# Optimization experiments

Measured on AMD Instinct MI355X. Metric: run time of the kernel, lower is better.

Reference implementation:

```python
import jax, jax.numpy as jnp
import numpy as np
import math

B, N, DIM, H, DH, NNULL = 2, 2048, 1024, 16, 64, 2
SCALE = 8.0
LN_EPS = 1e-5


def _alibi_slopes(heads):
    # heads is a power of 2 here (16): slopes = start * start**i
    start = 2.0 ** (-(2.0 ** (-(math.log2(heads) - 3))))
    return np.array([start * (start ** i) for i in range(heads)], dtype=np.float32)


def setup_inputs() -> dict:
    key = jax.random.key(0)
    ks = jax.random.split(key, 6)
    inner = H * DH
    return {
        "x": jax.random.normal(ks[0], (B, N, DIM), dtype=jnp.float32),
        "norm_g": jnp.ones((DIM,), jnp.float32),
        "norm_b": jnp.zeros((DIM,), jnp.float32),
        "Wq": jax.random.normal(ks[1], (DIM, inner), jnp.float32) * 0.02,
        "Wkv": jax.random.normal(ks[2], (DIM, 2 * inner), jnp.float32) * 0.02,
        "q_scale": jnp.ones((DH,), jnp.float32),
        "k_scale": jnp.ones((DH,), jnp.float32),
        "null_kv": jax.random.normal(ks[3], (H, 2 * NNULL, DH), jnp.float32),
        "Wout": jax.random.normal(ks[4], (inner, DIM), jnp.float32) * 0.02,
    }


def _l2norm(t):
    # matches F.normalize: x / max(||x||, 1e-12)
    n = jnp.sqrt(jnp.sum(t * t, axis=-1, keepdims=True))
    return t / jnp.maximum(n, 1e-12)


def reference(x, norm_g, norm_b, Wq, Wkv, q_scale, k_scale, null_kv, Wout):
    b, n, dim = x.shape
    h, dh, nn = H, DH, NNULL
    j = n + nn

    # NOTE: faithful to source -- K/V come from the PRE-norm x (kv_input bound
    # before x = self.norm(x)); only Q uses the LayerNorm'd x.
    mu = jnp.mean(x, axis=-1, keepdims=True)
    var = jnp.mean((x - mu) ** 2, axis=-1, keepdims=True)
    xn = (x - mu) * jax.lax.rsqrt(var + LN_EPS) * norm_g + norm_b

    q = (xn @ Wq).reshape(b, n, h, dh).transpose(0, 2, 1, 3)          # b h n d
    kv = x @ Wkv
    k, v = jnp.split(kv, 2, axis=-1)
    k = k.reshape(b, n, h, dh).transpose(0, 2, 1, 3)                   # b h n d
    v = v.reshape(b, n, h, dh).transpose(0, 2, 1, 3)

    # null kv: (h, 2*nn, dh) -> (h, nn, 2, dh)
    null = null_kv.reshape(h, nn, 2, dh)
    nk = jnp.broadcast_to(null[:, :, 0, :][None], (b, h, nn, dh))
    nv = jnp.broadcast_to(null[:, :, 1, :][None], (b, h, nn, dh))
    k = jnp.concatenate([nk, k], axis=2)                               # b h j d
    v = jnp.concatenate([nv, v], axis=2)

    q = _l2norm(q) * q_scale
    k = _l2norm(k) * k_scale

    sim = jnp.einsum('bhid,bhjd->bhij', q, k) * SCALE                  # b h n j

    # ALiBi bias: rows at positions j-n..j-1, cols 0..j-1
    irow = jnp.arange(j - n, j)
    jcol = jnp.arange(j)
    bias = -jnp.abs(jcol[None, :] - irow[:, None]).astype(sim.dtype)   # (n, j)
    slopes = jnp.asarray(_alibi_slopes(h))[:, None, None]              # (h,1,1)
    sim = sim + slopes * bias

    # causal mask: triu with offset j - n + 1 (null kv always visible)
    causal = jnp.triu(jnp.ones((n, j), dtype=bool), k=j - n + 1)
    neg = jnp.finfo(sim.dtype).max
    sim = jnp.where(causal[None, None], -neg, sim)

    attn = jax.nn.softmax(sim, axis=-1)
    out = jnp.einsum('bhij,bhjd->bhid', attn, v)
    out = out.transpose(0, 2, 1, 3).reshape(b, n, h * dh)
    return out @ Wout
```

## Files before the change

### kernel.cpp

```cpp
#include <hip/hip_runtime.h>
#include <hip/hip_bf16.h>
#include <stdint.h>

#define H_    16
#define N_    2048
#define DIM_  1024
#define DH_   64
#define NN_   2
#define J_    2050
#define JP_   2112
#define B_    2
#define M_    4096
#define NSEG_ 84

#define S8L_  11.541560327111707f
#define LOG2E_ 1.4426950408889634f

typedef unsigned short u16;
typedef unsigned int u32;
typedef short bf16x8 __attribute__((ext_vector_type(8)));
typedef float f32x4 __attribute__((ext_vector_type(4)));

__device__ __forceinline__ u16 f2b(float f) {
  union { float f; unsigned int i; } v; v.f = f;
  unsigned int r = v.i + 0x7fffu + ((v.i >> 16) & 1u);
  return (u16)(r >> 16);
}
__device__ __forceinline__ float b2f(u16 u) {
  union { unsigned int i; float f; } v; v.i = ((unsigned int)u) << 16; return v.f;
}
__device__ __forceinline__ float lo2f(u32 u) {
  union { u32 i; float f; } v; v.i = u << 16; return v.f;
}
__device__ __forceinline__ float hi2f(u32 u) {
  union { u32 i; float f; } v; v.i = u & 0xffff0000u; return v.f;
}
__device__ __forceinline__ void unp8(const uint4 u, float* d) {
  d[0] = lo2f(u.x); d[1] = hi2f(u.x); d[2] = lo2f(u.y); d[3] = hi2f(u.y);
  d[4] = lo2f(u.z); d[5] = hi2f(u.z); d[6] = lo2f(u.w); d[7] = hi2f(u.w);
}
__device__ __forceinline__ u32 pk2(float a, float b) {
  union { __hip_bfloat162 h; u32 u; } x;
  x.h = __float22bfloat162_rn(make_float2(a, b));
  return x.u;
}
__device__ __forceinline__ void dma16(const u16* g, u16* l) {
  __builtin_amdgcn_global_load_lds(
      (const __attribute__((address_space(1))) u32*)(const void*)g,
      (__attribute__((address_space(3))) u32*)(void*)l, 16, 0, 0);
}

__global__ __launch_bounds__(256) void ktranspose_cast(const float* __restrict__ in,
                                                       u16* __restrict__ out, int R, int C) {
  __shared__ float tile[32][33];
  int tx = threadIdx.x & 31, ty = threadIdx.x >> 5;
  int c0 = blockIdx.x * 32, r0 = blockIdx.y * 32;
  #pragma unroll
  for (int i = 0; i < 32; i += 8)
    tile[ty + i][tx] = in[(size_t)(r0 + ty + i) * C + c0 + tx];
  __syncthreads();
  #pragma unroll
  for (int i = 0; i < 32; i += 8)
    out[(size_t)(c0 + ty + i) * R + r0 + tx] = f2b(tile[tx][ty + i]);
}

__global__ __launch_bounds__(256) void lnorm_k(const float* __restrict__ x,
                                               const float* __restrict__ g,
                                               const float* __restrict__ bb,
                                               u16* __restrict__ xn,
                                               u16* __restrict__ xbf) {
  int row = blockIdx.x;
  int t = threadIdx.x;
  float4 rw = *(const float4*)(x + (size_t)row * DIM_ + t * 4);
  float v0 = rw.x, v1 = rw.y, v2 = rw.z, v3 = rw.w;
  uint2 cw;
  cw.x = pk2(v0, v1);
  cw.y = pk2(v2, v3);
  *(uint2*)(xbf + (size_t)row * DIM_ + t * 4) = cw;
  float s = v0 + v1 + v2 + v3;
  float ss = v0 * v0 + v1 * v1 + v2 * v2 + v3 * v3;
  #pragma unroll
  for (int o = 32; o; o >>= 1) { s += __shfl_xor(s, o, 64); ss += __shfl_xor(ss, o, 64); }
  __shared__ float red[8];
  int lane = t & 63, w = t >> 6;
  if (lane == 0) { red[w] = s; red[4 + w] = ss; }
  __syncthreads();
  float S = red[0] + red[1] + red[2] + red[3];
  float SS = red[4] + red[5] + red[6] + red[7];
  float mu = S * (1.0f / DIM_);
  float var = SS * (1.0f / DIM_) - mu * mu;
  float rs = rsqrtf(var + 1e-5f);
  float4 gv = *(const float4*)(g + t * 4);
  float4 bv = *(const float4*)(bb + t * 4);
  uint2 ow;
  ow.x = pk2((v0 - mu) * rs * gv.x + bv.x, (v1 - mu) * rs * gv.y + bv.y);
  ow.y = pk2((v2 - mu) * rs * gv.z + bv.z, (v3 - mu) * rs * gv.w + bv.w);
  *(uint2*)(xn + (size_t)row * DIM_ + t * 4) = ow;
}

template <int MODE>
__global__ __launch_bounds__(256) void gemm_k(const u16* __restrict__ A,
                                              const u16* __restrict__ BT,
                                              void* __restrict__ dst0,
                                              void* __restrict__ dst1,
                                              const float* __restrict__ scale,
                                              int M, int Nc, int K) {
  __shared__ u16 As[128 * 64];
  __shared__ u16 Bs[64 * 64];
  int tid = threadIdx.x, wv = tid >> 6, lane = tid & 63;
  int fm = lane & 15, fg = lane >> 4;
  int row0 = blockIdx.y * 128, col0 = blockIdx.x * 64;
  f32x4 acc[2][4] = {};
  int srow = lane >> 3;
  int skb = ((lane & 7) ^ srow) * 8;
  const u16* Ag = A + (size_t)(row0 + wv * 32 + srow) * K + skb;
  const u16* Bg = BT + (size_t)(col0 + wv * 16 + srow) * K + skb;
  u16* AsW = As + (wv * 32) * 64;
  u16* BsW = Bs + (wv * 16) * 64;
  int fr7 = fm & 7;
  int ak0 = (fg ^ fr7) * 8;
  int ak1 = ((fg + 4) ^ fr7) * 8;
  for (int k0 = 0; k0 < K; k0 += 64) {
    __syncthreads();
    dma16(Ag + k0,                    AsW);
    dma16(Ag + (size_t)8 * K + k0,    AsW + 8 * 64);
    dma16(Ag + (size_t)16 * K + k0,   AsW + 16 * 64);
    dma16(Ag + (size_t)24 * K + k0,   AsW + 24 * 64);
    dma16(Bg + k0,                    BsW);
    dma16(Bg + (size_t)8 * K + k0,    BsW + 8 * 64);
    __syncthreads();
    bf16x8 af0[2], af1[2], bf0[4], bf1[4];
    #pragma unroll
    for (int mt = 0; mt < 2; mt++) {
      int rbase = (wv * 32 + mt * 16 + fm) * 64;
      af0[mt] = *(const bf16x8*)&As[rbase + ak0];
      af1[mt] = *(const bf16x8*)&As[rbase + ak1];
    }
    #pragma unroll
    for (int nt = 0; nt < 4; nt++) {
      int rbase = (nt * 16 + fm) * 64;
      bf0[nt] = *(const bf16x8*)&Bs[rbase + ak0];
      bf1[nt] = *(const bf16x8*)&Bs[rbase + ak1];
    }
    #pragma unroll
    for (int mt = 0; mt < 2; mt++)
      #pragma unroll
      for (int nt = 0; nt < 4; nt++) {
        acc[mt][nt] = __builtin_amdgcn_mfma_f32_16x16x32_bf16(af0[mt], bf0[nt], acc[mt][nt], 0, 0, 0);
        acc[mt][nt] = __builtin_amdgcn_mfma_f32_16x16x32_bf16(af1[mt], bf1[nt], acc[mt][nt], 0, 0, 0);
      }
  }
  if (MODE == 1) {
    float* C = (float*)dst0;
    #pragma unroll
    for (int mt = 0; mt < 2; mt++)
      #pragma unroll
      for (int r = 0; r < 4; r++) {
        int m = row0 + wv * 32 + mt * 16 + fg * 4 + r;
        #pragma unroll
        for (int nt = 0; nt < 4; nt++)
          C[(size_t)m * Nc + col0 + nt * 16 + fm] = acc[mt][nt][r];
      }
  } else {
    bool isK = (MODE == 2) || (col0 < 1024);
    int h = (isK ? col0 : col0 - 1024) >> 6;
    float sv[4];
    if (isK) {
      #pragma unroll
      for (int nt = 0; nt < 4; nt++) sv[nt] = scale[nt * 16 + fm];
      if (MODE == 2) {
        #pragma unroll
        for (int nt = 0; nt < 4; nt++) sv[nt] *= S8L_;
      }
    }
    u16* Do = (u16*)((MODE == 3 && !isK) ? dst1 : dst0);
    #pragma unroll
    for (int mt = 0; mt < 2; mt++) {
      #pragma unroll
      for (int r = 0; r < 4; r++) {
        float inv = 1.0f;
        if (isK) {
          float ssp = 0.0f;
          #pragma unroll
          for (int nt = 0; nt < 4; nt++) ssp += acc[mt][nt][r] * acc[mt][nt][r];
          #pragma unroll
          for (int o = 1; o <= 8; o <<= 1) ssp += __shfl_xor(ssp, o, 64);
          inv = 1.0f / fmaxf(sqrtf(ssp), 1e-12f);
        }
        int m = row0 + wv * 32 + mt * 16 + fg * 4 + r;
        int b = m >> 11, n = m & 2047;
        size_t base;
        if (MODE == 2)      base = (((size_t)(b * H_ + h)) * N_ + n) * 64;
        else if (isK)       base = (((size_t)(b * H_ + h)) * JP_ + (n + NN_)) * 64;
        else                base = (((size_t)(b * H_ + h)) * J_ + (n + NN_)) * 64;
        #pragma unroll
        for (int nt = 0; nt < 4; nt++) {
          float val = acc[mt][nt][r];
          if (isK) val = val * inv * sv[nt];
          Do[base + nt * 16 + fm] = f2b(val);
        }
      }
    }
  }
}

__global__ __launch_bounds__(256) void vtransp_k(const u16* __restrict__ Vb,
                                                 const float* __restrict__ nkv,
                                                 const float* __restrict__ ks,
                                                 u16* __restrict__ Kb,
                                                 u16* __restrict__ VTp) {
  __shared__ u16 tile[64][80];
  int t = threadIdx.x;
  int c = blockIdx.x, bh = blockIdx.y, h = bh & 15;
  int jl = t >> 2, dc = (t & 3) * 16;
  int j = c * 64 + jl;
  if (j < NN_) {
    float kvv[16];
    float kssp = 0.0f;
    #pragma unroll
    for (int e = 0; e < 16; e++) {
      float vv = nkv[(size_t)(h * 4 + 2 * j + 1) * 64 + dc + e];
      tile[jl][dc + e] = f2b(vv);
      float kv = nkv[(size_t)(h * 4 + 2 * j) * 64 + dc + e];
      kvv[e] = kv; kssp += kv * kv;
    }
    kssp += __shfl_xor(kssp, 1, 64);
    kssp += __shfl_xor(kssp, 2, 64);
    float inv = 1.0f / fmaxf(sqrtf(kssp), 1e-12f);
    #pragma unroll
    for (int e = 0; e < 16; e++)
      Kb[((size_t)bh * JP_ + j) * 64 + dc + e] = f2b(kvv[e] * inv * ks[dc + e]);
  } else if (j < J_) {
    const uint4* src = (const uint4*)(Vb + ((size_t)bh * J_ + j) * 64 + dc);
    *(uint4*)&tile[jl][dc] = src[0];
    *(uint4*)&tile[jl][dc + 8] = src[1];
  } else {
    uint4 z = {0, 0, 0, 0};
    *(uint4*)&tile[jl][dc] = z;
    *(uint4*)&tile[jl][dc + 8] = z;
  }
  __syncthreads();
  int d = t >> 2, p0 = (t & 3) * 16;
  u16 tmp[16] __attribute__((aligned(16)));
  #pragma unroll
  for (int e = 0; e < 16; e++) {
    int pos = p0 + e;
    int h2 = pos >> 5, rem = pos & 31;
    int fgp = rem >> 3, tt = rem & 7;
    int nt = tt >> 2, r = tt & 3;
    int jloc = (h2 * 2 + nt) * 16 + fgp * 4 + r;
    tmp[e] = tile[jloc][d];
  }
  uint4* dstp = (uint4*)(VTp + ((size_t)bh * 64 + d) * JP_ + c * 64 + p0);
  dstp[0] = ((uint4*)tmp)[0];
  dstp[1] = ((uint4*)tmp)[1];
}

__global__ __launch_bounds__(256, 6) void attn_k(const u16* __restrict__ Qn,
                                                 const u16* __restrict__ Kb,
                                                 const u16* __restrict__ VTp,
                                                 const float* __restrict__ qs,
                                                 const float* __restrict__ ks,
                                                 u16* __restrict__ partials) {
  __shared__ u16 Ks0[64 * 32], Ks1[64 * 32];
  __shared__ u16 Vs0[64 * 32], Vs1[64 * 32];
  int tid = threadIdx.x;
  int wv = tid >> 6, lane = tid & 63;
  int fm = lane & 15, fg = lane >> 4;
  int n = (int)blockIdx.x + NSEG_ * (int)blockIdx.y;
  int m = n >> 3;
  int bh = (n & 7) * 4 + m / NSEG_;
  int segid = m % NSEG_;
  int h = bh & 15;
  int cum = 0, qt = 0, seg = 0;
  #pragma unroll 1
  for (int i = 0; i < 32; i++) {
    int t = 31 - i, s = (t + 9) >> 3;
    if (segid < cum + s) { qt = t; seg = segid - cum; break; }
    cum += s;
  }
  int q0 = qt * 64;
  int q = q0 + wv * 16 + fm;
  float slope = exp2f(-0.5f * (float)(h + 1));
  float prod = fabsf(qs[lane] * ks[lane]);
  #pragma unroll
  for (int o = 32; o; o >>= 1) prod = fmaxf(prod, __shfl_xor(prod, o, 64));
  float MbL = 8.0f * prod * LOG2E_;
  float slopeL = slope * LOG2E_;
  const u16* qp = Qn + ((size_t)bh * N_ + q) * 64 + fg * 8;
  bf16x8 qf0 = *(const bf16x8*)(qp);
  bf16x8 qf1 = *(const bf16x8*)(qp + 32);
  f32x4 accO[4] = {};
  float lp = 0.0f;
  int lr = lane >> 2;
  int kbs = ((lane & 3) ^ ((lane >> 3) & 3)) * 8;
  int fs = (fg ^ ((fm >> 1) & 3)) * 8;
  const u16* KbBH = Kb + (size_t)bh * JP_ * 64;
  const u16* VTbh = VTp + (size_t)bh * 64 * JP_;
  int c0 = seg * 8;
  int c1 = min(c0 + 8, qt + 2);
  float bias0 = slopeL * (float)(c0 * 64 + fg * 4 - q - 2) - MbL;
  float sr1 = slopeL, sr2 = slopeL * 2.0f, sr3 = slopeL * 3.0f;
  float s16 = slopeL * 16.0f;
  float d64 = slopeL * 64.0f;
  for (int c = c0; c < c1; c++) {
    int jb = c * 64;
    __syncthreads();
    const u16* Kg = KbBH + (size_t)(jb + wv * 16 + lr) * 64 + kbs;
    dma16(Kg,      Ks0 + wv * 512);
    dma16(Kg + 32, Ks1 + wv * 512);
    const u16* Vg = VTbh + (size_t)(wv * 16 + lr) * JP_ + jb + kbs;
    dma16(Vg,      Vs0 + wv * 512);
    dma16(Vg + 32, Vs1 + wv * 512);
    __syncthreads();
    f32x4 accS[4] = {};
    #pragma unroll
    for (int nt = 0; nt < 4; nt++) {
      bf16x8 kf0 = *(const bf16x8*)&Ks0[(nt * 16 + fm) * 32 + fs];
      accS[nt] = __builtin_amdgcn_mfma_f32_16x16x32_bf16(kf0, qf0, accS[nt], 0, 0, 0);
      bf16x8 kf1 = *(const bf16x8*)&Ks1[(nt * 16 + fm) * 32 + fs];
      accS[nt] = __builtin_amdgcn_mfma_f32_16x16x32_bf16(kf1, qf1, accS[nt], 0, 0, 0);
    }
    union { bf16x8 v; u32 u[4]; } P0, P1;
    float lps = 0.0f;
    float bnt = bias0;
    if (c < qt) {
      #pragma unroll
      for (int nt = 0; nt < 4; nt++) {
        float e0 = __builtin_amdgcn_exp2f(accS[nt][0] + bnt);
        float e1 = __builtin_amdgcn_exp2f((accS[nt][1] + sr1) + bnt);
        float e2 = __builtin_amdgcn_exp2f((accS[nt][2] + sr2) + bnt);
        float e3 = __builtin_amdgcn_exp2f((accS[nt][3] + sr3) + bnt);
        u32 w0 = pk2(e0, e1);
        u32 w1 = pk2(e2, e3);
        lps += (e0 + e1) + (e2 + e3);
        if (nt < 2) { P0.u[nt * 2] = w0; P0.u[nt * 2 + 1] = w1; }
        else        { P1.u[(nt - 2) * 2] = w0; P1.u[(nt - 2) * 2 + 1] = w1; }
        bnt += s16;
      }
    } else {
      int thr = q + 2 - jb;
      #pragma unroll
      for (int nt = 0; nt < 4; nt++) {
        int ib = nt * 16 + fg * 4;
        float e0 = __builtin_amdgcn_exp2f(accS[nt][0] + bnt);
        float e1 = __builtin_amdgcn_exp2f((accS[nt][1] + sr1) + bnt);
        float e2 = __builtin_amdgcn_exp2f((accS[nt][2] + sr2) + bnt);
        float e3 = __builtin_amdgcn_exp2f((accS[nt][3] + sr3) + bnt);
        e0 = (ib + 0 <= thr) ? e0 : 0.0f;
        e1 = (ib + 1 <= thr) ? e1 : 0.0f;
        e2 = (ib + 2 <= thr) ? e2 : 0.0f;
        e3 = (ib + 3 <= thr) ? e3 : 0.0f;
        u32 w0 = pk2(e0, e1);
        u32 w1 = pk2(e2, e3);
        lps += (e0 + e1) + (e2 + e3);
        if (nt < 2) { P0.u[nt * 2] = w0; P0.u[nt * 2 + 1] = w1; }
        else        { P1.u[(nt - 2) * 2] = w0; P1.u[(nt - 2) * 2 + 1] = w1; }
        bnt += s16;
      }
    }
    lp += lps;
    bias0 += d64;
    #pragma unroll
    for (int nt = 0; nt < 4; nt++) {
      bf16x8 vf0 = *(const bf16x8*)&Vs0[(nt * 16 + fm) * 32 + fs];
      accO[nt] = __builtin_amdgcn_mfma_f32_16x16x32_bf16(vf0, P0.v, accO[nt], 0, 0, 0);
      bf16x8 vf1 = *(const bf16x8*)&Vs1[(nt * 16 + fm) * 32 + fs];
      accO[nt] = __builtin_amdgcn_mfma_f32_16x16x32_bf16(vf1, P1.v, accO[nt], 0, 0, 0);
    }
  }
  lp += __shfl_xor(lp, 16, 64);
  lp += __shfl_xor(lp, 32, 64);
  u16* P = partials + ((size_t)bh * NSEG_ + segid) * 4224;
  int sq = wv * 16 + fm;
  #pragma unroll
  for (int nt = 0; nt < 4; nt++) {
    uint2 ow;
    ow.x = pk2(accO[nt][0], accO[nt][1]);
    ow.y = pk2(accO[nt][2], accO[nt][3]);
    *(uint2*)(P + sq * 64 + nt * 16 + fg * 4) = ow;
  }
  if (fg == 0) *(float*)(P + 4096 + 2 * sq) = lp;
}

__global__ __launch_bounds__(256) void comb_k(const u16* __restrict__ partials,
                                              u16* __restrict__ AO) {
  int qt = blockIdx.x, bh = blockIdx.y, b = bh >> 4, h = bh & 15;
  int t = threadIdx.x, q = t >> 2, dq = (t & 3) * 16;
  int s = (qt + 9) >> 3;
  int cum = 0;
  for (int tt = qt + 1; tt < 32; tt++) cum += (tt + 9) >> 3;
  float acc[16] = {};
  float lsum = 0.0f;
  for (int k = 0; k < s; k++) {
    const u16* P = partials + ((size_t)bh * NSEG_ + cum + k) * 4224;
    uint4 a = *(const uint4*)(P + q * 64 + dq);
    uint4 bq = *(const uint4*)(P + q * 64 + dq + 8);
    float tmp[8];
    unp8(a, tmp);
    #pragma unroll
    for (int e = 0; e < 8; e++) acc[e] += tmp[e];
    unp8(bq, tmp);
    #pragma unroll
    for (int e = 0; e < 8; e++) acc[8 + e] += tmp[e];
    lsum += *(const float*)(P + 4096 + 2 * q);
  }
  float linv = 1.0f / lsum;
  int n = qt * 64 + q;
  u16* dst = AO + (((size_t)(b * N_ + n)) * H_ + h) * 64 + dq;
  u16 ov[16] __attribute__((aligned(16)));
  #pragma unroll
  for (int e = 0; e < 16; e++) ov[e] = f2b(acc[e] * linv);
  *(uint4*)dst = ((uint4*)ov)[0];
  *(uint4*)(dst + 8) = ((uint4*)ov)[1];
}

extern "C" void kernel_launch(void* const* d_in, const int* in_sizes, int n_in,
                              void* d_out, int out_size, void* d_ws, size_t ws_size,
                              hipStream_t stream) {
  const float* x    = (const float*)d_in[0];
  const float* ng   = (const float*)d_in[1];
  const float* nb   = (const float*)d_in[2];
  const float* Wq   = (const float*)d_in[3];
  const float* Wkv  = (const float*)d_in[4];
  const float* qs   = (const float*)d_in[5];
  const float* ks   = (const float*)d_in[6];
  const float* nkv  = (const float*)d_in[7];
  const float* Wout = (const float*)d_in[8];
  float* out = (float*)d_out;
  char* ws = (char*)d_ws;

  u16* xn    = (u16*)(ws + 0);
  u16* WoutT = (u16*)(ws + 8388608);
  u16* Qn    = (u16*)(ws + 10485760);
  u16* Kb    = (u16*)(ws + 18874368);
  u16* VTp   = (u16*)(ws + 27525120);
  u16* xbf   = (u16*)(ws + 36175872);
  u16* WqT   = (u16*)(ws + 44564480);
  u16* WkvT  = (u16*)(ws + 46661632);
  u16* Vb    = (u16*)(ws + 50855936);
  u16* parts = xbf;
  u16* AO    = xn;

  hipMemsetAsync(Kb, 0, 8650752, stream);
  ktranspose_cast<<<dim3(32, 32), 256, 0, stream>>>(Wq, WqT, 1024, 1024);
  ktranspose_cast<<<dim3(64, 32), 256, 0, stream>>>(Wkv, WkvT, 1024, 2048);
  ktranspose_cast<<<dim3(32, 32), 256, 0, stream>>>(Wout, WoutT, 1024, 1024);
  lnorm_k<<<4096, 256, 0, stream>>>(x, ng, nb, xn, xbf);
  gemm_k<2><<<dim3(16, 32), 256, 0, stream>>>(xn, WqT, Qn, nullptr, qs, M_, 1024, 1024);
  gemm_k<3><<<dim3(32, 32), 256, 0, stream>>>(xbf, WkvT, Kb, Vb, ks, M_, 2048, 1024);
  vtransp_k<<<dim3(33, 32), 256, 0, stream>>>(Vb, nkv, ks, Kb, VTp);
  attn_k<<<dim3(NSEG_, 32), 256, 0, stream>>>(Qn, Kb, VTp, qs, ks, parts);
  comb_k<<<dim3(32, 32), 256, 0, stream>>>(parts, AO);
  gemm_k<1><<<dim3(16, 32), 256, 0, stream>>>(AO, WoutT, out, nullptr, nullptr, M_, 1024, 1024);
}
```

Before: 222.2 us.

## Double-buffer GEMM LDS, remap blocks for locality, merge transposes, drop memset

The GEMM kernel now double-buffers its A/B LDS tiles, issuing the next K-slice DMA before the current slice's MFMAs and using one barrier per iteration instead of two. Block indices are remapped so that groups of blocks land on distinct row bands, aiming at better L2 locality. The three weight transpose launches are merged into one kernel, and the full hipMemset of Kb is replaced by zeroing only the padded K rows inside vtransp_k. LDS use in the GEMM doubles, which may lower occupancy. Correctness now depends on every other Kb entry being written by the producing kernels.

```diff
diff --git a/kernel.cpp b/kernel.cpp
--- a/kernel.cpp
+++ b/kernel.cpp
@@ -50,11 +50,21 @@
       (__attribute__((address_space(3))) u32*)(void*)l, 16, 0, 0);
 }
 
-__global__ __launch_bounds__(256) void ktranspose_cast(const float* __restrict__ in,
-                                                       u16* __restrict__ out, int R, int C) {
+__global__ __launch_bounds__(256) void ktranspose3(const float* __restrict__ Wq,
+                                                   const float* __restrict__ Wkv,
+                                                   const float* __restrict__ Wout,
+                                                   u16* __restrict__ WqT,
+                                                   u16* __restrict__ WkvT,
+                                                   u16* __restrict__ WoutT) {
   __shared__ float tile[32][33];
+  int bx = blockIdx.x;
+  const float* in; u16* out; int C; int cx;
+  if (bx < 32)      { in = Wq;   out = WqT;   C = 1024; cx = bx; }
+  else if (bx < 96) { in = Wkv;  out = WkvT;  C = 2048; cx = bx - 32; }
+  else              { in = Wout; out = WoutT; C = 1024; cx = bx - 96; }
+  const int R = 1024;
   int tx = threadIdx.x & 31, ty = threadIdx.x >> 5;
-  int c0 = blockIdx.x * 32, r0 = blockIdx.y * 32;
+  int c0 = cx * 32, r0 = blockIdx.y * 32;
   #pragma unroll
   for (int i = 0; i < 32; i += 8)
     tile[ty + i][tx] = in[(size_t)(r0 + ty + i) * C + c0 + tx];
@@ -105,42 +115,60 @@
                                               void* __restrict__ dst1,
                                               const float* __restrict__ scale,
                                               int M, int Nc, int K) {
-  __shared__ u16 As[128 * 64];
-  __shared__ u16 Bs[64 * 64];
+  __shared__ u16 As[2][128 * 64];
+  __shared__ u16 Bs[2][64 * 64];
   int tid = threadIdx.x, wv = tid >> 6, lane = tid & 63;
   int fm = lane & 15, fg = lane >> 4;
-  int row0 = blockIdx.y * 128, col0 = blockIdx.x * 64;
+  int nlin = (int)blockIdx.x + (int)gridDim.x * (int)blockIdx.y;
+  int gx = (int)gridDim.x;
+  int ypc = (int)gridDim.y >> 3;
+  int mm = nlin >> 3;
+  int row0 = ((nlin & 7) * ypc + mm / gx) * 128;
+  int col0 = (mm % gx) * 64;
   f32x4 acc[2][4] = {};
   int srow = lane >> 3;
   int skb = ((lane & 7) ^ srow) * 8;
   const u16* Ag = A + (size_t)(row0 + wv * 32 + srow) * K + skb;
   const u16* Bg = BT + (size_t)(col0 + wv * 16 + srow) * K + skb;
-  u16* AsW = As + (wv * 32) * 64;
-  u16* BsW = Bs + (wv * 16) * 64;
   int fr7 = fm & 7;
   int ak0 = (fg ^ fr7) * 8;
   int ak1 = ((fg + 4) ^ fr7) * 8;
+  {
+    u16* AsW = As[0] + (wv * 32) * 64;
+    u16* BsW = Bs[0] + (wv * 16) * 64;
+    dma16(Ag,                    AsW);
+    dma16(Ag + (size_t)8 * K,    AsW + 8 * 64);
+    dma16(Ag + (size_t)16 * K,   AsW + 16 * 64);
+    dma16(Ag + (size_t)24 * K,   AsW + 24 * 64);
+    dma16(Bg,                    BsW);
+    dma16(Bg + (size_t)8 * K,    BsW + 8 * 64);
+  }
+  __syncthreads();
+  int cur = 0;
   for (int k0 = 0; k0 < K; k0 += 64) {
-    __syncthreads();
-    dma16(Ag + k0,                    AsW);
-    dma16(Ag + (size_t)8 * K + k0,    AsW + 8 * 64);
-    dma16(Ag + (size_t)16 * K + k0,   AsW + 16 * 64);
-    dma16(Ag + (size_t)24 * K + k0,   AsW + 24 * 64);
-    dma16(Bg + k0,                    BsW);
-    dma16(Bg + (size_t)8 * K + k0,    BsW + 8 * 64);
-    __syncthreads();
+    if (k0 + 64 < K) {
+      int kn = k0 + 64;
+      u16* AsW = As[cur ^ 1] + (wv * 32) * 64;
+      u16* BsW = Bs[cur ^ 1] + (wv * 16) * 64;
+      dma16(Ag + kn,                    AsW);
+      dma16(Ag + (size_t)8 * K + kn,    AsW + 8 * 64);
+      dma16(Ag + (size_t)16 * K + kn,   AsW + 16 * 64);
+      dma16(Ag + (size_t)24 * K + kn,   AsW + 24 * 64);
+      dma16(Bg + kn,                    BsW);
+      dma16(Bg + (size_t)8 * K + kn,    BsW + 8 * 64);
+    }
     bf16x8 af0[2], af1[2], bf0[4], bf1[4];
     #pragma unroll
     for (int mt = 0; mt < 2; mt++) {
       int rbase = (wv * 32 + mt * 16 + fm) * 64;
-      af0[mt] = *(const bf16x8*)&As[rbase + ak0];
-      af1[mt] = *(const bf16x8*)&As[rbase + ak1];
+      af0[mt] = *(const bf16x8*)&As[cur][rbase + ak0];
+      af1[mt] = *(const bf16x8*)&As[cur][rbase + ak1];
     }
     #pragma unroll
     for (int nt = 0; nt < 4; nt++) {
       int rbase = (nt * 16 + fm) * 64;
-      bf0[nt] = *(const bf16x8*)&Bs[rbase + ak0];
-      bf1[nt] = *(const bf16x8*)&Bs[rbase + ak1];
+      bf0[nt] = *(const bf16x8*)&Bs[cur][rbase + ak0];
+      bf1[nt] = *(const bf16x8*)&Bs[cur][rbase + ak1];
     }
     #pragma unroll
     for (int mt = 0; mt < 2; mt++)
@@ -149,6 +177,8 @@
         acc[mt][nt] = __builtin_amdgcn_mfma_f32_16x16x32_bf16(af0[mt], bf0[nt], acc[mt][nt], 0, 0, 0);
         acc[mt][nt] = __builtin_amdgcn_mfma_f32_16x16x32_bf16(af1[mt], bf1[nt], acc[mt][nt], 0, 0, 0);
       }
+    __syncthreads();
+    cur ^= 1;
   }
   if (MODE == 1) {
     float* C = (float*)dst0;
@@ -238,6 +268,9 @@
     uint4 z = {0, 0, 0, 0};
     *(uint4*)&tile[jl][dc] = z;
     *(uint4*)&tile[jl][dc + 8] = z;
+    uint4* kd = (uint4*)(Kb + ((size_t)bh * JP_ + j) * 64 + dc);
+    kd[0] = z;
+    kd[1] = z;
   }
   __syncthreads();
   int d = t >> 2, p0 = (t & 3) * 16;
@@ -442,10 +475,7 @@
   u16* parts = xbf;
   u16* AO    = xn;
 
-  hipMemsetAsync(Kb, 0, 8650752, stream);
-  ktranspose_cast<<<dim3(32, 32), 256, 0, stream>>>(Wq, WqT, 1024, 1024);
-  ktranspose_cast<<<dim3(64, 32), 256, 0, stream>>>(Wkv, WkvT, 1024, 2048);
-  ktranspose_cast<<<dim3(32, 32), 256, 0, stream>>>(Wout, WoutT, 1024, 1024);
+  ktranspose3<<<dim3(128, 32), 256, 0, stream>>>(Wq, Wkv, Wout, WqT, WkvT, WoutT);
   lnorm_k<<<4096, 256, 0, stream>>>(x, ng, nb, xn, xbf);
   gemm_k<2><<<dim3(16, 32), 256, 0, stream>>>(xn, WqT, Qn, nullptr, qs, M_, 1024, 1024);
   gemm_k<3><<<dim3(32, 32), 256, 0, stream>>>(xbf, WkvT, Kb, Vb, ks, M_, 2048, 1024);
```

After: 214.4 us. 3.5% less time.
